# Optimization experiments

Hardware: AMD Instinct MI355X
Metric: run time of the kernel (lower is better)

Reference implementation:

```python
import jax, jax.numpy as jnp
import numpy as np

B, H, W = 16, 1024, 1024
BOUNDARY_WEIGHT = 2.0
FOCAL_ALPHA = 0.25
FOCAL_GAMMA = 2.0
SMOOTH = 1e-6


def setup_inputs() -> dict:
    key = jax.random.key(0)
    k1, k2, k3 = jax.random.split(key, 3)
    pred_masks = jax.random.normal(k1, (B, 1, H, W), dtype=jnp.float32)
    gt_masks = jax.random.bernoulli(k2, 0.5, (B, 1, H, W)).astype(jnp.float32)
    pred_iou = jax.random.uniform(k3, (B, 1), dtype=jnp.float32)
    return {"pred_masks": pred_masks, "gt_masks": gt_masks, "pred_iou": pred_iou}


def _bce_with_logits(x, t):
    # stable: softplus(x) - x*t == -[t*log(sig(x)) + (1-t)*log(1-sig(x))]
    return jax.nn.softplus(x) - x * t


def reference(pred_masks, gt_masks, pred_iou):
    x, t = pred_masks, gt_masks
    ce = _bce_with_logits(x, t)                      # (B,1,H,W)
    p = jax.nn.sigmoid(x)

    # focal loss
    p_t = p * t + (1.0 - p) * (1.0 - t)
    alpha_t = FOCAL_ALPHA * t + (1.0 - FOCAL_ALPHA) * (1.0 - t)
    focal = jnp.mean(alpha_t * ce * (1.0 - p_t) ** FOCAL_GAMMA)

    # dice loss
    intersection = jnp.sum(p * t, axis=(2, 3))       # (B,1)
    union = jnp.sum(p, axis=(2, 3)) + jnp.sum(t, axis=(2, 3))
    dice = 1.0 - jnp.mean((2.0 * intersection + SMOOTH) / (union + SMOOTH))

    # boundary-weighted BCE. In the source, dist = EDT(mask) is 0 at every
    # background pixel and dist_inv = EDT(1-mask) is 0 at every foreground
    # pixel, so min(dist, dist_inv) == 0 <= 3 at EVERY pixel -> the weight
    # map is uniformly boundary_weight. Faithful equivalent:
    boundary = BOUNDARY_WEIGHT * jnp.mean(ce)

    total = focal + dice + 0.5 * boundary

    # IoU auxiliary loss (thresholded prediction; no grad flows through >0.5)
    pred_bin = (p > 0.5).astype(x.dtype)
    inter = jnp.sum(pred_bin * t, axis=(1, 2, 3))    # (B,)
    uni = jnp.sum(pred_bin, axis=(1, 2, 3)) + jnp.sum(t, axis=(1, 2, 3)) - inter
    actual_iou = (inter + SMOOTH) / (uni + SMOOTH)
    iou_loss = jnp.mean((jnp.squeeze(pred_iou) - actual_iou) ** 2)

    return total + 0.1 * iou_loss
```

## Files before the change

### kernel.cpp

```cpp
#include <hip/hip_runtime.h>
#include <math.h>


#define HW_PIX (1024 * 1024)
#define BATCH 16
constexpr int BLOCKS_PER_IMG = 128;
constexpr int THREADS = 256;
constexpr int PIX_PER_BLOCK = HW_PIX / BLOCKS_PER_IMG;
constexpr int ITERS = PIX_PER_BLOCK / (THREADS * 4);

__global__ __launch_bounds__(THREADS) void
loss_partial(const float* __restrict__ x, const float* __restrict__ t,
             float* __restrict__ acc) {
  const int b = blockIdx.x / BLOCKS_PER_IMG;
  const int chunk = blockIdx.x % BLOCKS_PER_IMG;
  const long base = (long)b * HW_PIX + (long)chunk * PIX_PER_BLOCK;
  const float4* __restrict__ x4 = (const float4*)(x + base);
  const float4* __restrict__ t4 = (const float4*)(t + base);

  float fsum = 0.f, csum = 0.f, isum = 0.f, psum = 0.f, tsum = 0.f,
        bisum = 0.f, bpsum = 0.f;

#pragma unroll
  for (int i = 0; i < ITERS; ++i) {
    float4 xv = x4[threadIdx.x + i * THREADS];
    float4 tv = t4[threadIdx.x + i * THREADS];
    const float* xs = reinterpret_cast<const float*>(&xv);
    const float* ts = reinterpret_cast<const float*>(&tv);
#pragma unroll
    for (int j = 0; j < 4; ++j) {
      const float xx = xs[j];
      const float tt = ts[j];
      const float e = __expf(-fabsf(xx));
      const float r = __builtin_amdgcn_rcpf(1.0f + e);
      const float p = (xx >= 0.0f) ? r : e * r;
      const float ce = fmaxf(xx, 0.0f) - xx * tt + __logf(1.0f + e);
      const float om = p + tt - 2.0f * p * tt;
      const float at = 0.75f - 0.5f * tt;
      fsum += at * ce * om * om;
      csum += ce;
      isum += p * tt;
      psum += p;
      tsum += tt;
      const float bin = (xx > 0.0f) ? 1.0f : 0.0f;
      bisum += bin * tt;
      bpsum += bin;
    }
  }

  float vals[7] = {fsum, csum, isum, psum, tsum, bisum, bpsum};
  __shared__ float red[THREADS / 64][7];
  const int lane = threadIdx.x & 63;
  const int wave = threadIdx.x >> 6;
#pragma unroll
  for (int k = 0; k < 7; ++k) {
    float v = vals[k];
#pragma unroll
    for (int off = 32; off > 0; off >>= 1) v += __shfl_down(v, off);
    if (lane == 0) red[wave][k] = v;
  }
  __syncthreads();
  if (threadIdx.x < 7) {
    const float s = red[0][threadIdx.x] + red[1][threadIdx.x] +
                    red[2][threadIdx.x] + red[3][threadIdx.x];
    atomicAdd(&acc[b * 7 + threadIdx.x], s);
  }
}

__global__ void loss_final(const float* __restrict__ acc,
                           const float* __restrict__ pred_iou,
                           float* __restrict__ out) {
  constexpr float SMOOTH = 1e-6f;
  const int lane = threadIdx.x;
  float F = 0.f, C = 0.f, D = 0.f, Q = 0.f;
  if (lane < BATCH) {
    const float* a = acc + lane * 7;
    F = a[0];
    C = a[1];
    const float I = a[2], P = a[3], T = a[4], BI = a[5], BP = a[6];
    D = (2.0f * I + SMOOTH) / (P + T + SMOOTH);
    const float iou = (BI + SMOOTH) / (BP + T - BI + SMOOTH);
    const float d = pred_iou[lane] - iou;
    Q = d * d;
  }
#pragma unroll
  for (int off = 32; off > 0; off >>= 1) {
    F += __shfl_down(F, off);
    C += __shfl_down(C, off);
    D += __shfl_down(D, off);
    Q += __shfl_down(Q, off);
  }
  if (lane == 0) {
    const float invN = 1.0f / (float)((long)BATCH * HW_PIX);
    const float focal = F * invN;
    const float dice = 1.0f - D * (1.0f / (float)BATCH);
    const float half_boundary = C * invN;
    const float iou_loss = Q * (1.0f / (float)BATCH);
    out[0] = focal + dice + half_boundary + 0.1f * iou_loss;
  }
}

extern "C" void kernel_launch(void* const* d_in, const int* in_sizes, int n_in,
                              void* d_out, int out_size, void* d_ws,
                              size_t ws_size, hipStream_t stream) {
  const float* x = (const float*)d_in[0];
  const float* t = (const float*)d_in[1];
  const float* piou = (const float*)d_in[2];
  float* acc = (float*)d_ws;

  hipMemsetAsync(acc, 0, BATCH * 7 * sizeof(float), stream);
  loss_partial<<<BATCH * BLOCKS_PER_IMG, THREADS, 0, stream>>>(x, t, acc);
  loss_final<<<1, 64, 0, stream>>>(acc, piou, (float*)d_out);
}
```

Measured before the change: 155.2 us.

## Preload all tiles, use wave ballots for counts, double block count

Issues all float4 loads for a thread up front so more memory requests are in flight before compute begins, and doubles the number of blocks per image. The three binary sums (target count, thresholded prediction count, their intersection) are now computed with wave-wide ballots and popcounts, which removes their per-thread accumulation and three cross-lane shuffle reductions. The extra blocks double the atomic traffic, and holding every tile in registers raises register pressure. Exact integer counts stand in for float sums, which is equivalent for 0/1 targets.

```diff
diff --git a/kernel.cpp b/kernel.cpp
--- a/kernel.cpp
+++ b/kernel.cpp
@@ -4,7 +4,7 @@
 
 #define HW_PIX (1024 * 1024)
 #define BATCH 16
-constexpr int BLOCKS_PER_IMG = 128;
+constexpr int BLOCKS_PER_IMG = 256;
 constexpr int THREADS = 256;
 constexpr int PIX_PER_BLOCK = HW_PIX / BLOCKS_PER_IMG;
 constexpr int ITERS = PIX_PER_BLOCK / (THREADS * 4);
@@ -18,46 +18,58 @@
   const float4* __restrict__ x4 = (const float4*)(x + base);
   const float4* __restrict__ t4 = (const float4*)(t + base);
 
-  float fsum = 0.f, csum = 0.f, isum = 0.f, psum = 0.f, tsum = 0.f,
-        bisum = 0.f, bpsum = 0.f;
+  float4 xv[ITERS], tv[ITERS];
+#pragma unroll
+  for (int i = 0; i < ITERS; ++i) {
+    xv[i] = x4[threadIdx.x + i * THREADS];
+    tv[i] = t4[threadIdx.x + i * THREADS];
+  }
+
+  float fsum = 0.f, csum = 0.f, isum = 0.f, psum = 0.f;
+  unsigned tcnt = 0, bicnt = 0, bpcnt = 0;
 
 #pragma unroll
   for (int i = 0; i < ITERS; ++i) {
-    float4 xv = x4[threadIdx.x + i * THREADS];
-    float4 tv = t4[threadIdx.x + i * THREADS];
-    const float* xs = reinterpret_cast<const float*>(&xv);
-    const float* ts = reinterpret_cast<const float*>(&tv);
+    const float* xs = reinterpret_cast<const float*>(&xv[i]);
+    const float* ts = reinterpret_cast<const float*>(&tv[i]);
 #pragma unroll
     for (int j = 0; j < 4; ++j) {
       const float xx = xs[j];
       const float tt = ts[j];
       const float e = __expf(-fabsf(xx));
-      const float r = __builtin_amdgcn_rcpf(1.0f + e);
+      const float s = 1.0f + e;
+      const float r = __builtin_amdgcn_rcpf(s);
       const float p = (xx >= 0.0f) ? r : e * r;
-      const float ce = fmaxf(xx, 0.0f) - xx * tt + __logf(1.0f + e);
-      const float om = p + tt - 2.0f * p * tt;
+      const float ce = fmaxf(xx, 0.0f) - xx * tt + __logf(s);
+      const float om = fmaf(tt, 1.0f - 2.0f * p, p);
       const float at = 0.75f - 0.5f * tt;
       fsum += at * ce * om * om;
       csum += ce;
-      isum += p * tt;
+      isum = fmaf(p, tt, isum);
       psum += p;
-      tsum += tt;
-      const float bin = (xx > 0.0f) ? 1.0f : 0.0f;
-      bisum += bin * tt;
-      bpsum += bin;
+      const unsigned long long mt = __ballot(tt != 0.0f);
+      const unsigned long long mb = __ballot(xx > 0.0f);
+      tcnt  += (unsigned)__popcll(mt);
+      bpcnt += (unsigned)__popcll(mb);
+      bicnt += (unsigned)__popcll(mt & mb);
     }
   }
 
-  float vals[7] = {fsum, csum, isum, psum, tsum, bisum, bpsum};
   __shared__ float red[THREADS / 64][7];
   const int lane = threadIdx.x & 63;
   const int wave = threadIdx.x >> 6;
+  float vals[4] = {fsum, csum, isum, psum};
 #pragma unroll
-  for (int k = 0; k < 7; ++k) {
+  for (int k = 0; k < 4; ++k) {
     float v = vals[k];
 #pragma unroll
     for (int off = 32; off > 0; off >>= 1) v += __shfl_down(v, off);
     if (lane == 0) red[wave][k] = v;
+  }
+  if (lane == 0) {
+    red[wave][4] = (float)tcnt;
+    red[wave][5] = (float)bicnt;
+    red[wave][6] = (float)bpcnt;
   }
   __syncthreads();
   if (threadIdx.x < 7) {
```

New measurement: 151.6 us. 1.02x faster.
